# Kernel tuning notes

Measured on AMD Instinct MI355X. Metric: run time of the kernel, lower is better.

## Reference

```python
import jax, jax.numpy as jnp
import numpy as np

EPS = 1e-05  # matches tf entropy epsilon


def setup_inputs() -> dict:
    key = jax.random.key(0)
    k1, k2 = jax.random.split(key)
    encodings = jax.random.normal(k1, (8192, 64), dtype=jnp.float32)
    categorical = jax.random.uniform(k2, (8192, 25), dtype=jnp.float32)
    return {"encodings": encodings, "categorical": categorical, "k": 15}


def reference(encodings, categorical, k):
    B = encodings.shape[0]
    n_components = categorical.shape[1]
    k = min(k, B // 4)  # layer clamps k to batch_size // 4

    hard_groups = jnp.argmax(categorical, axis=1)           # [B] int
    max_groups = jnp.max(categorical, axis=1)               # [B]

    # Batched brute-force kNN. tf.norm's sqrt is monotonic, so the strict
    # comparison `dist < kth_dist` is identical on squared distances; working
    # in squared space avoids sqrt(0) issues and an extra pass.
    sq = jnp.sum(encodings * encodings, axis=1)             # [B]
    d2 = sq[:, None] + sq[None, :] - 2.0 * (encodings @ encodings.T)
    d2 = jnp.maximum(d2, 0.0)                               # [B, B]

    # (k+1)-smallest distances per row (0-indexed k, self-distance included,
    # matching tf.gather(tf.sort(distances), k)).
    neg_topk, _ = jax.lax.top_k(-d2, k + 1)                 # [B, k+1]
    kth = -neg_topk[:, k]                                   # [B] k-th smallest

    mask = (d2 < kth[:, None]).astype(jnp.float32)          # [B, B] strict <

    # Per-row label histogram over the neighborhood: counts[i,c] = #neighbors
    # of i in cluster c. Zero bins contribute 0 to -sum(b*log(b+eps)), same as
    # tf.bincount's variable-length output.
    onehot = jax.nn.one_hot(hard_groups, n_components, dtype=jnp.float32)
    counts = mask @ onehot                                  # [B, n_components]
    n_i = jnp.sum(counts, axis=-1, keepdims=True)           # [B, 1]
    bins = counts / jnp.maximum(n_i, 1.0)
    neighbourhood_entropy = -jnp.sum(bins * jnp.log(bins + EPS), axis=-1)  # [B]

    # Global cluster-size entropy + number of populated clusters.
    gcounts = jnp.sum(onehot, axis=0)                       # [n_components]
    gbins = gcounts / jnp.float32(B)
    cluster_size_entropy = -jnp.sum(gbins * jnp.log(gbins + EPS))
    n_populated = jnp.sum(gcounts > 0).astype(jnp.float32)

    return encodings, neighbourhood_entropy, cluster_size_entropy, n_populated, max_groups
```

## Files before the change

kernel.cpp:

```cpp
#include <hip/hip_runtime.h>
#include <math.h>

#define Bsz    8192
#define Dd     64
#define NC     25
#define RT     64
#define JT     64
#define SPLITS 8
#define TILES  (Bsz / SPLITS / JT)
#define KCAP   16
#define RSU    136
#define EPSf   1e-5f

typedef short  short8  __attribute__((ext_vector_type(8)));
typedef float  floatx4 __attribute__((ext_vector_type(4)));

#define GLD16(g, l) __builtin_amdgcn_global_load_lds((const __attribute__((address_space(1))) unsigned int*)(g), \
                     (__attribute__((address_space(3))) unsigned int*)(l), 16, 0, 0)
#define GLD4(g, l)  __builtin_amdgcn_global_load_lds((const __attribute__((address_space(1))) unsigned int*)(g), \
                     (__attribute__((address_space(3))) unsigned int*)(l), 4, 0, 0)

__device__ inline unsigned short f2bf(float x) {
    unsigned u = __float_as_uint(x);
    u += 0x7FFFu + ((u >> 16) & 1u);
    return (unsigned short)(u >> 16);
}
__device__ inline float bf2f(unsigned short h) { return __uint_as_float(((unsigned)h) << 16); }

__device__ inline void bsort16(unsigned* a) {
    #pragma unroll
    for (int k = 2; k <= 16; k <<= 1)
        #pragma unroll
        for (int j = k >> 1; j > 0; j >>= 1)
            #pragma unroll
            for (int i = 0; i < 16; ++i) {
                int l = i ^ j;
                if (l > i) {
                    bool up = ((i & k) == 0) || (k == 16);
                    unsigned x = a[i], y = a[l];
                    unsigned lo = (x < y) ? x : y, hi = (x < y) ? y : x;
                    a[i] = up ? lo : hi;
                    a[l] = up ? hi : lo;
                }
            }
}
__device__ inline void bclean16(unsigned* t) {
    #pragma unroll
    for (int j = 8; j > 0; j >>= 1)
        #pragma unroll
        for (int i = 0; i < 16; ++i) {
            int l = i ^ j;
            if (l > i) {
                unsigned x = t[i], y = t[l];
                t[i] = (x < y) ? x : y;
                t[l] = (x < y) ? y : x;
            }
        }
}
__device__ inline void bmerge16(unsigned* ls, const unsigned* b) {
    unsigned t[16];
    #pragma unroll
    for (int i = 0; i < 16; ++i) { unsigned x = ls[i], y = b[15 - i]; t[i] = (x < y) ? x : y; }
    bclean16(t);
    #pragma unroll
    for (int i = 0; i < 16; ++i) ls[i] = t[i];
}
__device__ inline void bmerge16_shfl(unsigned* ls, int mask) {
    unsigned t[16];
    #pragma unroll
    for (int i = 0; i < 16; ++i) {
        unsigned pv = (unsigned)__shfl_xor((int)ls[15 - i], mask);
        unsigned x = ls[i];
        t[i] = (x < pv) ? x : pv;
    }
    bclean16(t);
    #pragma unroll
    for (int i = 0; i < 16; ++i) ls[i] = t[i];
}


__global__ __launch_bounds__(256) void pre_kernel(
    const float* __restrict__ enc, const float* __restrict__ cat,
    unsigned int* __restrict__ slab,
    unsigned short* __restrict__ enc1, unsigned short* __restrict__ enc2,
    float* __restrict__ out_max, float* __restrict__ out_enc)
{
    const int gid = blockIdx.x * 256 + threadIdx.x;
    const int p = gid >> 5, pr = gid & 31;

    ((float2*)out_enc)[gid] = ((const float2*)enc)[gid];

    float2 ev = ((const float2*)(enc + p * Dd))[pr];
    float s = ev.x * ev.x + ev.y * ev.y;
    #pragma unroll
    for (int m = 1; m < 32; m <<= 1) s += __shfl_xor(s, m, 32);

    {
        unsigned* d1 = (unsigned*)(enc1 + (size_t)p * RSU);
        unsigned* d2 = (unsigned*)(enc2 + (size_t)p * RSU);
        unsigned short ha = f2bf(ev.x), hb = f2bf(ev.y);
        unsigned short la = f2bf(ev.x - bf2f(ha)), lb = f2bf(ev.y - bf2f(hb));
        d1[pr]      = (unsigned)ha | ((unsigned)hb << 16);
        d1[32 + pr] = (unsigned)la | ((unsigned)lb << 16);
        float y0 = -2.f * ev.x, y1 = -2.f * ev.y;
        unsigned short hc = f2bf(y0), hd = f2bf(y1);
        unsigned short lc = f2bf(y0 - bf2f(hc)), ld = f2bf(y1 - bf2f(hd));
        d2[pr]      = (unsigned)hc | ((unsigned)hd << 16);
        d2[32 + pr] = (unsigned)lc | ((unsigned)ld << 16);
    }
    float cv = (pr < NC) ? cat[p * NC + pr] : -1.f;
    int ci = pr;
    #pragma unroll
    for (int m = 1; m < 32; m <<= 1) {
        float ov = __shfl_xor(cv, m, 32);
        int   oi = __shfl_xor(ci, m, 32);
        if (ov > cv || (ov == cv && oi < ci)) { cv = ov; ci = oi; }
    }
    if (pr == 0) {
        out_max[p] = cv;
        slab[p] = (__float_as_uint(s) & ~31u) | (unsigned)ci;
    }
}

__global__ __launch_bounds__(256, 4) void main_kernel(
    const unsigned short* __restrict__ enc1, const unsigned short* __restrict__ enc2,
    const unsigned int* __restrict__ slab, unsigned int* __restrict__ lists)
{
    __shared__ __align__(16) unsigned short Ai[RT * RSU];
    __shared__ __align__(16) unsigned short Bj[JT * RSU];
    __shared__ __align__(16) unsigned int   slds[JT];

    const int tid  = threadIdx.x;
    const int wv   = tid >> 6, lane = tid & 63;
    const int quad = (tid >> 4) & 3, c15 = tid & 15;
    const int rowgrp = blockIdx.x >> 3, s = blockIdx.x & 7;
    const int rowbase = rowgrp * RT;
    const int jb0 = s * (Bsz / SPLITS);

    {
        const char* gi = (const char*)(enc1 + (size_t)rowbase * RSU);
        const char* gj = (const char*)(enc2 + (size_t)jb0 * RSU);
        char* li = (char*)Ai; char* lj = (char*)Bj;
        for (int c = wv; c < 17; c += 4) GLD16(gi + c * 1024 + lane * 16, li + c * 1024 + lane * 16);
        for (int c = wv; c < 17; c += 4) GLD16(gj + c * 1024 + lane * 16, lj + c * 1024 + lane * 16);
        if (wv == 3) GLD4((const char*)(slab + jb0) + lane * 4, (char*)slds + lane * 4);
    }
    const float sqi = __uint_as_float(slab[rowbase + 16 * wv + c15] & ~31u);
    __syncthreads();

    short8 bh[2], bl[2];
    #pragma unroll
    for (int c = 0; c < 2; ++c) {
        bh[c] = *(const short8*)&Ai[(16 * wv + c15) * RSU + quad * 8 + c * 32];
        bl[c] = *(const short8*)&Ai[(16 * wv + c15) * RSU + 64 + quad * 8 + c * 32];
    }

    unsigned int ls[KCAP];
    #pragma unroll
    for (int q = 0; q < KCAP; ++q) ls[q] = 0xFFFFFFFFu;

    for (int t = 0; t < TILES; ++t) {
        floatx4 acc[4];
        #pragma unroll
        for (int nt = 0; nt < 4; ++nt) acc[nt] = (floatx4){0.f, 0.f, 0.f, 0.f};
        #pragma unroll
        for (int nt = 0; nt < 4; ++nt) {
            #pragma unroll
            for (int c = 0; c < 2; ++c) {
                short8 ah = *(const short8*)&Bj[(16 * nt + c15) * RSU + quad * 8 + c * 32];
                short8 al = *(const short8*)&Bj[(16 * nt + c15) * RSU + 64 + quad * 8 + c * 32];
                acc[nt] = __builtin_amdgcn_mfma_f32_16x16x32_bf16(ah, bh[c], acc[nt], 0, 0, 0);
                acc[nt] = __builtin_amdgcn_mfma_f32_16x16x32_bf16(ah, bl[c], acc[nt], 0, 0, 0);
                acc[nt] = __builtin_amdgcn_mfma_f32_16x16x32_bf16(al, bh[c], acc[nt], 0, 0, 0);
            }
        }
        unsigned cand[16];
        #pragma unroll
        for (int nt = 0; nt < 4; ++nt) {
            uint4 sv = *(const uint4*)&slds[16 * nt + 4 * quad];
            unsigned slr[4] = {sv.x, sv.y, sv.z, sv.w};
            #pragma unroll
            for (int r = 0; r < 4; ++r) {
                unsigned sl = slr[r];
                float d2 = fmaxf(sqi + __uint_as_float(sl & ~31u) + acc[nt][r], 0.f);
                cand[4 * nt + r] = (__float_as_uint(d2) & ~31u) | (sl & 31u);
            }
        }
        __syncthreads();
        if (t + 1 < TILES) {
            const char* gj = (const char*)(enc2 + (size_t)(jb0 + (t + 1) * JT) * RSU);
            char* lj = (char*)Bj;
            for (int c = wv; c < 17; c += 4) GLD16(gj + c * 1024 + lane * 16, lj + c * 1024 + lane * 16);
            if (wv == 3) GLD4((const char*)(slab + jb0 + (t + 1) * JT) + lane * 4, (char*)slds + lane * 4);
        }
        bsort16(cand);
        bmerge16(ls, cand);
        __syncthreads();
    }

    bmerge16_shfl(ls, 16);
    bmerge16_shfl(ls, 32);
    if (quad == 0) {
        uint4* outl = (uint4*)(lists + ((unsigned)(rowbase + 16 * wv + c15) * SPLITS + s) * KCAP);
        outl[0] = make_uint4(ls[0],  ls[1],  ls[2],  ls[3]);
        outl[1] = make_uint4(ls[4],  ls[5],  ls[6],  ls[7]);
        outl[2] = make_uint4(ls[8],  ls[9],  ls[10], ls[11]);
        outl[3] = make_uint4(ls[12], ls[13], ls[14], ls[15]);
    }
}

__global__ __launch_bounds__(256) void merge_kernel(
    const unsigned int* __restrict__ lists, const int* __restrict__ kptr,
    const unsigned int* __restrict__ slab,
    float* __restrict__ out_ent, float* __restrict__ out_glob)
{
    __shared__ int cnt[32];
    const int g = blockIdx.x * 256 + threadIdx.x;
    const int row = g >> 2, sub = g & 3;

    unsigned A[16], Bv[16];
    {
        const uint4* src = (const uint4*)(lists + (unsigned)row * (SPLITS * KCAP) + sub * 32);
        #pragma unroll
        for (int i = 0; i < 4; ++i) {
            uint4 v = src[i];
            A[4*i] = v.x; A[4*i+1] = v.y; A[4*i+2] = v.z; A[4*i+3] = v.w;
        }
        #pragma unroll
        for (int i = 0; i < 4; ++i) {
            uint4 v = src[4 + i];
            Bv[4*i] = v.x; Bv[4*i+1] = v.y; Bv[4*i+2] = v.z; Bv[4*i+3] = v.w;
        }
    }
    bmerge16(A, Bv);
    bmerge16_shfl(A, 1);
    bmerge16_shfl(A, 2);

    int kk = kptr[0];
    if (kk > Bsz / 4) kk = Bsz / 4;
    if (kk > KCAP - 1) kk = KCAP - 1;

    unsigned kth = A[15];
    #pragma unroll
    for (int q = 0; q < 16; ++q) if (q == kk) kth = A[q];
    int nn = 0;
    #pragma unroll
    for (int t = 0; t < 15; ++t) nn += (t < kk && A[t] < kth) ? 1 : 0;

    float inv = 1.f / (float)((nn > 0) ? nn : 1);
    float part = 0.f;
    #pragma unroll
    for (int a4 = 0; a4 < 4; ++a4) {
        int a = sub + 4 * a4;
        if (a < nn) {
            int la = (int)(A[a] & 31u);
            int c = 0;
            #pragma unroll
            for (int b = 0; b < 15; ++b) c += (b < nn && (int)(A[b] & 31u) == la) ? 1 : 0;
            part -= inv * logf((float)c * inv + EPSf);
        }
    }
    part += __shfl_xor(part, 1);
    part += __shfl_xor(part, 2);
    if (sub == 0) out_ent[row] = part;

    if (blockIdx.x == 0) {
        const int tid = threadIdx.x;
        if (tid < 32) cnt[tid] = 0;
        __syncthreads();
        for (int i = tid; i < Bsz; i += 256) atomicAdd(&cnt[slab[i] & 31u], 1);
        __syncthreads();
        if (tid == 0) {
            float gent = 0.f, npop = 0.f;
            for (int i = 0; i < NC; ++i) {
                int gcv = cnt[i];
                if (gcv > 0) {
                    npop += 1.f;
                    float gb = (float)gcv / (float)Bsz;
                    gent -= gb * logf(gb + EPSf);
                }
            }
            out_glob[0] = gent;
            out_glob[1] = npop;
        }
    }
}

extern "C" void kernel_launch(void* const* d_in, const int* in_sizes, int n_in,
                              void* d_out, int out_size, void* d_ws, size_t ws_size,
                              hipStream_t stream)
{
    const float* enc  = (const float*)d_in[0];
    const float* cat  = (const float*)d_in[1];
    const int*   kptr = (const int*)d_in[2];
    float* out = (float*)d_out;

    unsigned int*   slab  = (unsigned int*)d_ws;
    unsigned short* enc1  = (unsigned short*)((char*)d_ws + 32768);
    unsigned short* enc2  = (unsigned short*)((char*)d_ws + 2260992);
    unsigned int*   lists = (unsigned int*)((char*)d_ws + 4489216);

    float* out_enc  = out;
    float* out_ent  = out + Bsz * Dd;
    float* out_glob = out + Bsz * Dd + Bsz;
    float* out_max  = out + Bsz * Dd + Bsz + 2;

    pre_kernel<<<1024, 256, 0, stream>>>(enc, cat, slab, enc1, enc2, out_max, out_enc);
    main_kernel<<<(Bsz / RT) * SPLITS, 256, 0, stream>>>(enc1, enc2, slab, lists);
    merge_kernel<<<128, 256, 0, stream>>>(lists, kptr, slab, out_ent, out_glob);
}
```

Before: 129.5 us.

## Fuse merge stage into main kernel via last-block-per-rowgroup atomic ticket

Removes the separate merge kernel launch. Each main_kernel block writes its partial top-16 lists with atomic exchanges, then bumps a per-rowgroup counter. The last of the 8 split blocks for a rowgroup reads the lists back with atomics, merges them and computes the neighbourhood entropy. Rowgroup 0 also computes the global histogram. This saves a launch and its gap, but adds atomic traffic, a dummy store to keep ordering, and a serialized tail on the finishing blocks.

After: 147.8 us. 14.2% more time.

```diff
diff --git a/kernel.cpp b/kernel.cpp
--- a/kernel.cpp
+++ b/kernel.cpp
@@ -81,12 +81,14 @@
 
 __global__ __launch_bounds__(256) void pre_kernel(
     const float* __restrict__ enc, const float* __restrict__ cat,
-    unsigned int* __restrict__ slab,
+    int* __restrict__ grp_tick, unsigned int* __restrict__ slab,
     unsigned short* __restrict__ enc1, unsigned short* __restrict__ enc2,
     float* __restrict__ out_max, float* __restrict__ out_enc)
 {
     const int gid = blockIdx.x * 256 + threadIdx.x;
     const int p = gid >> 5, pr = gid & 31;
+
+    if (blockIdx.x == 0 && threadIdx.x < 128) grp_tick[threadIdx.x] = 0;
 
     ((float2*)out_enc)[gid] = ((const float2*)enc)[gid];
 
@@ -124,11 +126,14 @@
 
 __global__ __launch_bounds__(256, 4) void main_kernel(
     const unsigned short* __restrict__ enc1, const unsigned short* __restrict__ enc2,
-    const unsigned int* __restrict__ slab, unsigned int* __restrict__ lists)
+    const unsigned int* __restrict__ slab, unsigned int* __restrict__ lists,
+    int* __restrict__ grp_tick, const int* __restrict__ kptr,
+    float* __restrict__ out_ent, float* __restrict__ out_glob)
 {
     __shared__ __align__(16) unsigned short Ai[RT * RSU];
     __shared__ __align__(16) unsigned short Bj[JT * RSU];
     __shared__ __align__(16) unsigned int   slds[JT];
+    __shared__ int winflag_s;
 
     const int tid  = threadIdx.x;
     const int wv   = tid >> 6, lane = tid & 63;
@@ -200,72 +205,64 @@
 
     bmerge16_shfl(ls, 16);
     bmerge16_shfl(ls, 32);
-    if (quad == 0) {
-        uint4* outl = (uint4*)(lists + ((unsigned)(rowbase + 16 * wv + c15) * SPLITS + s) * KCAP);
-        outl[0] = make_uint4(ls[0],  ls[1],  ls[2],  ls[3]);
-        outl[1] = make_uint4(ls[4],  ls[5],  ls[6],  ls[7]);
-        outl[2] = make_uint4(ls[8],  ls[9],  ls[10], ls[11]);
-        outl[3] = make_uint4(ls[12], ls[13], ls[14], ls[15]);
-    }
-}
-
-__global__ __launch_bounds__(256) void merge_kernel(
-    const unsigned int* __restrict__ lists, const int* __restrict__ kptr,
-    const unsigned int* __restrict__ slab,
-    float* __restrict__ out_ent, float* __restrict__ out_glob)
-{
-    __shared__ int cnt[32];
-    const int g = blockIdx.x * 256 + threadIdx.x;
-    const int row = g >> 2, sub = g & 3;
-
-    unsigned A[16], Bv[16];
+    unsigned dummy = 0;
     {
-        const uint4* src = (const uint4*)(lists + (unsigned)row * (SPLITS * KCAP) + sub * 32);
-        #pragma unroll
-        for (int i = 0; i < 4; ++i) {
-            uint4 v = src[i];
-            A[4*i] = v.x; A[4*i+1] = v.y; A[4*i+2] = v.z; A[4*i+3] = v.w;
-        }
-        #pragma unroll
-        for (int i = 0; i < 4; ++i) {
-            uint4 v = src[4 + i];
-            Bv[4*i] = v.x; Bv[4*i+1] = v.y; Bv[4*i+2] = v.z; Bv[4*i+3] = v.w;
-        }
-    }
-    bmerge16(A, Bv);
-    bmerge16_shfl(A, 1);
-    bmerge16_shfl(A, 2);
-
-    int kk = kptr[0];
-    if (kk > Bsz / 4) kk = Bsz / 4;
-    if (kk > KCAP - 1) kk = KCAP - 1;
-
-    unsigned kth = A[15];
-    #pragma unroll
-    for (int q = 0; q < 16; ++q) if (q == kk) kth = A[q];
-    int nn = 0;
-    #pragma unroll
-    for (int t = 0; t < 15; ++t) nn += (t < kk && A[t] < kth) ? 1 : 0;
-
-    float inv = 1.f / (float)((nn > 0) ? nn : 1);
-    float part = 0.f;
-    #pragma unroll
-    for (int a4 = 0; a4 < 4; ++a4) {
-        int a = sub + 4 * a4;
-        if (a < nn) {
-            int la = (int)(A[a] & 31u);
-            int c = 0;
-            #pragma unroll
-            for (int b = 0; b < 15; ++b) c += (b < nn && (int)(A[b] & 31u) == la) ? 1 : 0;
-            part -= inv * logf((float)c * inv + EPSf);
-        }
-    }
-    part += __shfl_xor(part, 1);
-    part += __shfl_xor(part, 2);
-    if (sub == 0) out_ent[row] = part;
-
-    if (blockIdx.x == 0) {
-        const int tid = threadIdx.x;
+        unsigned* outl = lists + ((unsigned)(rowbase + 16 * wv + c15) * SPLITS + s) * KCAP;
+        #pragma unroll
+        for (int j = 0; j < 4; ++j)
+            dummy |= atomicExch(&outl[4 * quad + j], ls[4 * quad + j]);
+    }
+    __syncthreads();
+    if (tid == 0) {
+        grp_tick[128 + (int)(dummy & 127u)] = (int)dummy;
+        winflag_s = (atomicAdd(&grp_tick[rowgrp], 1) == SPLITS - 1);
+    }
+    __syncthreads();
+    if (!winflag_s) return;
+
+    {
+        const int row = rowbase + (tid >> 2), sub = tid & 3;
+        unsigned A[16], Bv[16];
+        unsigned* src = lists + (unsigned)row * (SPLITS * KCAP) + sub * 32;
+        #pragma unroll
+        for (int i = 0; i < 16; ++i) A[i] = atomicOr(&src[i], 0u);
+        #pragma unroll
+        for (int i = 0; i < 16; ++i) Bv[i] = atomicOr(&src[16 + i], 0u);
+        bmerge16(A, Bv);
+        bmerge16_shfl(A, 1);
+        bmerge16_shfl(A, 2);
+
+        int kk = kptr[0];
+        if (kk > Bsz / 4) kk = Bsz / 4;
+        if (kk > KCAP - 1) kk = KCAP - 1;
+
+        unsigned kth = A[15];
+        #pragma unroll
+        for (int q = 0; q < 16; ++q) if (q == kk) kth = A[q];
+        int nn = 0;
+        #pragma unroll
+        for (int t = 0; t < 15; ++t) nn += (t < kk && A[t] < kth) ? 1 : 0;
+
+        float inv = 1.f / (float)((nn > 0) ? nn : 1);
+        float part = 0.f;
+        #pragma unroll
+        for (int a4 = 0; a4 < 4; ++a4) {
+            int a = sub + 4 * a4;
+            if (a < nn) {
+                int la = (int)(A[a] & 31u);
+                int c = 0;
+                #pragma unroll
+                for (int b = 0; b < 15; ++b) c += (b < nn && (int)(A[b] & 31u) == la) ? 1 : 0;
+                part -= inv * logf((float)c * inv + EPSf);
+            }
+        }
+        part += __shfl_xor(part, 1);
+        part += __shfl_xor(part, 2);
+        if (sub == 0) out_ent[row] = part;
+    }
+
+    if (rowgrp == 0) {
+        int* cnt = (int*)slds;
         if (tid < 32) cnt[tid] = 0;
         __syncthreads();
         for (int i = tid; i < Bsz; i += 256) atomicAdd(&cnt[slab[i] & 31u], 1);
@@ -273,10 +270,10 @@
         if (tid == 0) {
             float gent = 0.f, npop = 0.f;
             for (int i = 0; i < NC; ++i) {
-                int gcv = cnt[i];
-                if (gcv > 0) {
+                int g = cnt[i];
+                if (g > 0) {
                     npop += 1.f;
-                    float gb = (float)gcv / (float)Bsz;
+                    float gb = (float)g / (float)Bsz;
                     gent -= gb * logf(gb + EPSf);
                 }
             }
@@ -295,17 +292,19 @@
     const int*   kptr = (const int*)d_in[2];
     float* out = (float*)d_out;
 
-    unsigned int*   slab  = (unsigned int*)d_ws;
-    unsigned short* enc1  = (unsigned short*)((char*)d_ws + 32768);
-    unsigned short* enc2  = (unsigned short*)((char*)d_ws + 2260992);
-    unsigned int*   lists = (unsigned int*)((char*)d_ws + 4489216);
+    int*            grp_tick = (int*)d_ws;
+    unsigned int*   slab     = (unsigned int*)((char*)d_ws + 4096);
+    unsigned short* enc1     = (unsigned short*)((char*)d_ws + 36864);
+    unsigned short* enc2     = (unsigned short*)((char*)d_ws + 2265088);
+    unsigned int*   lists    = (unsigned int*)((char*)d_ws + 4493312);
 
     float* out_enc  = out;
     float* out_ent  = out + Bsz * Dd;
     float* out_glob = out + Bsz * Dd + Bsz;
     float* out_max  = out + Bsz * Dd + Bsz + 2;
 
-    pre_kernel<<<1024, 256, 0, stream>>>(enc, cat, slab, enc1, enc2, out_max, out_enc);
-    main_kernel<<<(Bsz / RT) * SPLITS, 256, 0, stream>>>(enc1, enc2, slab, lists);
-    merge_kernel<<<128, 256, 0, stream>>>(lists, kptr, slab, out_ent, out_glob);
-}
+    pre_kernel<<<1024, 256, 0, stream>>>(enc, cat, grp_tick, slab, enc1, enc2,
+                                         out_max, out_enc);
+    main_kernel<<<(Bsz / RT) * SPLITS, 256, 0, stream>>>(enc1, enc2, slab, lists,
+                                                         grp_tick, kptr, out_ent, out_glob);
+}
```
